# Kernel optimization log

Hardware: AMD Instinct MI355X
Metric: run time of the kernel (lower is better)

Reference implementation:

```python
import jax, jax.numpy as jnp
import numpy as np

IN_FT = 256
OUT_FT = 256


def setup_inputs() -> dict:
    key = jax.random.key(0)
    k1, k2, k3 = jax.random.split(key, 3)
    B, N = 4, 4096
    seq = jax.random.normal(k1, (B, N, IN_FT), dtype=jnp.float32)
    adj = jax.random.uniform(k2, (B, N, N), dtype=jnp.float32)
    # Xavier-uniform fc weight [out_ft, in_ft], bias zeros
    limit = float(np.sqrt(6.0 / (IN_FT + OUT_FT)))
    W = jax.random.uniform(k3, (OUT_FT, IN_FT), minval=-limit, maxval=limit, dtype=jnp.float32)
    b = jnp.zeros((OUT_FT,), dtype=jnp.float32)
    alpha = jnp.array(0.25, dtype=jnp.float32)  # PReLU shared parameter
    return {"seq": seq, "adj": adj, "W": W, "b": b, "alpha": alpha}


def reference(seq, adj, W, b, alpha):
    # Linear projection: [B, N, out_ft]
    h = jnp.einsum("bni,oi->bno", seq, W) + b
    # Neighbor aggregation (dense bmm path): [B, N, N] @ [B, N, out_ft]
    h = jnp.einsum("bnm,bmo->bno", adj, h)
    # PReLU with shared alpha
    return jnp.where(h > 0, h, alpha * h)
```

## Files before the change

### kernel.cpp

```cpp
#include <hip/hip_runtime.h>
#include <hip/hip_bf16.h>

#define NSEQ 4096
#define FT 256
#define BK 64
#define NT (NSEQ / BK)

typedef __attribute__((ext_vector_type(8))) short bf16x8;
typedef __attribute__((ext_vector_type(4))) float f32x4;

__device__ __forceinline__ ushort f2bf(float f) {
  __hip_bfloat16 h = __float2bfloat16(f);
  return *reinterpret_cast<const ushort*>(&h);
}

__device__ __forceinline__ int swz(int row, int byteInRow) {
  return row * 128 + (byteInRow ^ ((row & 7) << 4));
}

__device__ __forceinline__ void mma_step(const char* lAp, const char* lBp,
                                         int lane, int wm, int wn,
                                         f32x4 acc[2][4]) {
  const int r16 = lane & 15;
  const int g16 = (lane >> 4) * 16;
#pragma unroll
  for (int kk = 0; kk < 2; ++kk) {
    const int kb = kk * 64 + g16;
    bf16x8 a[2], b[4];
#pragma unroll
    for (int mi = 0; mi < 2; ++mi) {
      const int row = wm * 32 + mi * 16 + r16;
      a[mi] = *reinterpret_cast<const bf16x8*>(lAp + swz(row, kb));
    }
#pragma unroll
    for (int ni = 0; ni < 4; ++ni) {
      const int row = wn * 64 + ni * 16 + r16;
      b[ni] = *reinterpret_cast<const bf16x8*>(lBp + swz(row, kb));
    }
#pragma unroll
    for (int mi = 0; mi < 2; ++mi)
#pragma unroll
      for (int ni = 0; ni < 4; ++ni)
        acc[mi][ni] = __builtin_amdgcn_mfma_f32_16x16x32_bf16(a[mi], b[ni],
                                                             acc[mi][ni], 0, 0, 0);
  }
}

__global__ __launch_bounds__(512) void linear_kernel(
    const float* __restrict__ seq, const float* __restrict__ W,
    const float* __restrict__ bias, ushort* __restrict__ hT) {
  __shared__ __align__(16) ushort lA[2][64 * 64];
  __shared__ __align__(16) ushort lB[2][256 * 64];

  const int tid = threadIdx.x;
  const int lane = tid & 63;
  const int wid = tid >> 6;
  const int wm = wid >> 2, wn = wid & 3;
  const int m0 = blockIdx.x * 64;

  const int ar = tid >> 4, ac = tid & 15;

  f32x4 rA[2];
  f32x4 rB[8];

  auto gload = [&](int t) {
    const int k0 = t * BK;
#pragma unroll
    for (int p = 0; p < 2; ++p)
      rA[p] = *reinterpret_cast<const f32x4*>(
          seq + (size_t)(m0 + ar + p * 32) * FT + k0 + ac * 4);
#pragma unroll
    for (int p = 0; p < 8; ++p)
      rB[p] = *reinterpret_cast<const f32x4*>(
          W + (size_t)(ar + p * 32) * FT + k0 + ac * 4);
  };
  auto lwrite = [&](int buf) {
    char* lAp = (char*)lA[buf];
    char* lBp = (char*)lB[buf];
#pragma unroll
    for (int p = 0; p < 2; ++p) {
      ushort4 u = make_ushort4(f2bf(rA[p][0]), f2bf(rA[p][1]), f2bf(rA[p][2]), f2bf(rA[p][3]));
      *reinterpret_cast<ushort4*>(lAp + swz(ar + p * 32, ac * 8)) = u;
    }
#pragma unroll
    for (int p = 0; p < 8; ++p) {
      ushort4 u = make_ushort4(f2bf(rB[p][0]), f2bf(rB[p][1]), f2bf(rB[p][2]), f2bf(rB[p][3]));
      *reinterpret_cast<ushort4*>(lBp + swz(ar + p * 32, ac * 8)) = u;
    }
  };

  f32x4 acc[2][4];
  const f32x4 zero = {0.f, 0.f, 0.f, 0.f};
#pragma unroll
  for (int mi = 0; mi < 2; ++mi)
#pragma unroll
    for (int ni = 0; ni < 4; ++ni) acc[mi][ni] = zero;

  gload(0);
  lwrite(0);
  const int NTA = FT / BK;
  for (int t = 0; t < NTA; ++t) {
    const int cur = t & 1;
    __syncthreads();
    if (t + 1 < NTA) gload(t + 1);
    mma_step((const char*)lA[cur], (const char*)lB[cur], lane, wm, wn, acc);
    if (t + 1 < NTA) lwrite(cur ^ 1);
  }

#pragma unroll
  for (int mi = 0; mi < 2; ++mi) {
    const int grow = m0 + wm * 32 + mi * 16 + ((lane >> 4) << 2);
    const int batch = grow >> 12;
    const int n = grow & (NSEQ - 1);
#pragma unroll
    for (int ni = 0; ni < 4; ++ni) {
      const int o = wn * 64 + ni * 16 + (lane & 15);
      const float bo = bias[o];
      ushort4 u;
      u.x = f2bf(acc[mi][ni][0] + bo);
      u.y = f2bf(acc[mi][ni][1] + bo);
      u.z = f2bf(acc[mi][ni][2] + bo);
      u.w = f2bf(acc[mi][ni][3] + bo);
      *reinterpret_cast<ushort4*>(hT + (size_t)(batch * FT + o) * NSEQ + n) = u;
    }
  }
}

__global__ __launch_bounds__(512) void bmm_prelu_kernel(
    const float* __restrict__ adj, const ushort* __restrict__ hT,
    const float* __restrict__ alphaP, float* __restrict__ out) {
  __shared__ __align__(16) ushort lA[2][64 * 64];
  __shared__ __align__(16) ushort lB[4][256 * 64];

  const int tid = threadIdx.x;
  const int lane = tid & 63;
  const int wid = tid >> 6;
  const int wm = wid >> 2, wn = wid & 3;

  const int bid = blockIdx.x;
  const int sbid = (bid & 7) * 32 + (bid >> 3);
  const int batch = sbid >> 6;
  const int m0 = (sbid & 63) * 64;

  const float* adjB = adj + (size_t)batch * NSEQ * NSEQ + (size_t)m0 * NSEQ;
  const ushort* hTB = hT + (size_t)batch * FT * NSEQ;

  const int ar = tid >> 4, ac = tid & 15;
  const int brow = wid * 8 + (lane >> 3);
  const int bg = (lane & 7) ^ (lane >> 3);

  f32x4 rA0[2], rA1[2], rA2[2], rA3[2];

  f32x4 acc[2][4];
  const f32x4 zero = {0.f, 0.f, 0.f, 0.f};
#pragma unroll
  for (int mi = 0; mi < 2; ++mi)
#pragma unroll
    for (int ni = 0; ni < 4; ++ni) acc[mi][ni] = zero;

  auto issueA = [&](int t, f32x4* r) {
    const int k0 = t * BK;
#pragma unroll
    for (int p = 0; p < 2; ++p)
      r[p] = *reinterpret_cast<const f32x4*>(
          adjB + (size_t)(ar + p * 32) * NSEQ + k0 + ac * 4);
  };
  auto issueB = [&](int t, int ib) {
    const int k0 = t * BK;
#pragma unroll
    for (int p = 0; p < 4; ++p) {
      const ushort* gp = hTB + (size_t)(p * 64 + brow) * NSEQ + k0 + bg * 8;
      ushort* lp = &lB[ib][p * 4096 + wid * 512];
      __builtin_amdgcn_global_load_lds(
          (const __attribute__((address_space(1))) void*)gp,
          (__attribute__((address_space(3))) void*)lp, 16, 0, 0);
    }
  };
  auto writeA = [&](const f32x4* r, int ia) {
    char* lAp = (char*)lA[ia];
#pragma unroll
    for (int p = 0; p < 2; ++p) {
      ushort4 u = make_ushort4(f2bf(r[p][0]), f2bf(r[p][1]), f2bf(r[p][2]), f2bf(r[p][3]));
      *reinterpret_cast<ushort4*>(lAp + swz(ar + p * 32, ac * 8)) = u;
    }
  };

  issueA(0, rA0);
  issueB(0, 0);
  issueA(1, rA1);
  issueB(1, 1);
  issueA(2, rA2);
  issueB(2, 2);
  asm volatile("s_waitcnt vmcnt(16)" ::: "memory");
  writeA(rA0, 0);
  asm volatile("s_waitcnt vmcnt(12) lgkmcnt(0)" ::: "memory");
  __builtin_amdgcn_s_barrier();
  __builtin_amdgcn_sched_barrier(0);

  auto body = [&](int t, f32x4* rIss, const f32x4* rWr,
                  int ibIss, int ibRd, int iaRd, int iaWr) {
    issueA(t + 3, rIss);
    issueB(t + 3, ibIss);
    __builtin_amdgcn_s_setprio(1);
    mma_step((const char*)lA[iaRd], (const char*)lB[ibRd], lane, wm, wn, acc);
    __builtin_amdgcn_s_setprio(0);
    asm volatile("s_waitcnt vmcnt(12)" ::: "memory");
    writeA(rWr, iaWr);
    asm volatile("s_waitcnt lgkmcnt(0)" ::: "memory");
    __builtin_amdgcn_s_barrier();
    __builtin_amdgcn_sched_barrier(0);
  };

  for (int j = 0; j < 15; ++j) {
    body(j * 4 + 0, rA3, rA1, 3, 0, 0, 1);
    body(j * 4 + 1, rA0, rA2, 0, 1, 1, 0);
    body(j * 4 + 2, rA1, rA3, 1, 2, 0, 1);
    body(j * 4 + 3, rA2, rA0, 2, 3, 1, 0);
  }
  body(60, rA3, rA1, 3, 0, 0, 1);
  {
    __builtin_amdgcn_s_setprio(1);
    mma_step((const char*)lA[1], (const char*)lB[1], lane, wm, wn, acc);
    __builtin_amdgcn_s_setprio(0);
    asm volatile("s_waitcnt vmcnt(6)" ::: "memory");
    writeA(rA2, 0);
    asm volatile("s_waitcnt lgkmcnt(0)" ::: "memory");
    __builtin_amdgcn_s_barrier();
    __builtin_amdgcn_sched_barrier(0);
  }
  {
    __builtin_amdgcn_s_setprio(1);
    mma_step((const char*)lA[0], (const char*)lB[2], lane, wm, wn, acc);
    __builtin_amdgcn_s_setprio(0);
    asm volatile("s_waitcnt vmcnt(0)" ::: "memory");
    writeA(rA3, 1);
    asm volatile("s_waitcnt lgkmcnt(0)" ::: "memory");
    __builtin_amdgcn_s_barrier();
    __builtin_amdgcn_sched_barrier(0);
  }
  mma_step((const char*)lA[1], (const char*)lB[3], lane, wm, wn, acc);

  const float alpha = *alphaP;
  __syncthreads();
  float* lo = (float*)&lB[0][0];
  const int PITCH = 264;
#pragma unroll
  for (int mi = 0; mi < 2; ++mi) {
    const int rbase = wm * 32 + mi * 16 + ((lane >> 4) << 2);
#pragma unroll
    for (int ni = 0; ni < 4; ++ni) {
      const int o = wn * 64 + ni * 16 + (lane & 15);
#pragma unroll
      for (int j = 0; j < 4; ++j) {
        float v = acc[mi][ni][j];
        v = v > 0.f ? v : alpha * v;
        lo[(rbase + j) * PITCH + o] = v;
      }
    }
  }
  __syncthreads();
  float* outB = out + ((size_t)batch * NSEQ + m0) * FT;
  const int r = tid >> 3, c8 = tid & 7;
#pragma unroll
  for (int k = 0; k < 8; ++k) {
    const int g = c8 + k * 8;
    f32x4 v = *reinterpret_cast<const f32x4*>(lo + r * PITCH + g * 4);
    __builtin_nontemporal_store(v, reinterpret_cast<f32x4*>(outB + (size_t)r * FT + g * 4));
  }
}

extern "C" void kernel_launch(void* const* d_in, const int* in_sizes, int n_in,
                              void* d_out, int out_size, void* d_ws, size_t ws_size,
                              hipStream_t stream) {
  const float* seq = (const float*)d_in[0];
  const float* adj = (const float*)d_in[1];
  const float* W = (const float*)d_in[2];
  const float* bias = (const float*)d_in[3];
  const float* alpha = (const float*)d_in[4];
  float* out = (float*)d_out;
  ushort* hT = (ushort*)d_ws;

  linear_kernel<<<256, 512, 0, stream>>>(seq, W, bias, hT);
  bmm_prelu_kernel<<<256, 512, 0, stream>>>(adj, hT, alpha, out);
}
```

Measured before the change: 90.51 us.

## Switch bmm to BK=128 tiles with double buffering instead of 4-stage BK=64

```diff
diff --git a/kernel.cpp b/kernel.cpp
--- a/kernel.cpp
+++ b/kernel.cpp
@@ -4,7 +4,8 @@
 #define NSEQ 4096
 #define FT 256
 #define BK 64
-#define NT (NSEQ / BK)
+#define BKB 128
+#define NTB (NSEQ / BKB)
 
 typedef __attribute__((ext_vector_type(8))) short bf16x8;
 typedef __attribute__((ext_vector_type(4))) float f32x4;
@@ -129,8 +130,7 @@
 __global__ __launch_bounds__(512) void bmm_prelu_kernel(
     const float* __restrict__ adj, const ushort* __restrict__ hT,
     const float* __restrict__ alphaP, float* __restrict__ out) {
-  __shared__ __align__(16) ushort lA[2][64 * 64];
-  __shared__ __align__(16) ushort lB[4][256 * 64];
+  __shared__ __align__(16) char smem[2 * 65536 + 2 * 16384];
 
   const int tid = threadIdx.x;
   const int lane = tid & 63;
@@ -145,11 +145,13 @@
   const float* adjB = adj + (size_t)batch * NSEQ * NSEQ + (size_t)m0 * NSEQ;
   const ushort* hTB = hT + (size_t)batch * FT * NSEQ;
 
-  const int ar = tid >> 4, ac = tid & 15;
-  const int brow = wid * 8 + (lane >> 3);
-  const int bg = (lane & 7) ^ (lane >> 3);
-
-  f32x4 rA0[2], rA1[2], rA2[2], rA3[2];
+  auto lB = [&](int i) -> char* { return smem + i * 65536; };
+  auto lA = [&](int i) -> char* { return smem + 131072 + i * 16384; };
+
+  const int arow = tid >> 3, ac = tid & 7;
+  const int bro = (lane >> 4);
+  const int bhalf = (lane >> 3) & 1;
+  f32x4 rS[4];
 
   f32x4 acc[2][4];
   const f32x4 zero = {0.f, 0.f, 0.f, 0.f};
@@ -158,91 +160,105 @@
 #pragma unroll
     for (int ni = 0; ni < 4; ++ni) acc[mi][ni] = zero;
 
-  auto issueA = [&](int t, f32x4* r) {
-    const int k0 = t * BK;
-#pragma unroll
-    for (int p = 0; p < 2; ++p)
-      r[p] = *reinterpret_cast<const f32x4*>(
-          adjB + (size_t)(ar + p * 32) * NSEQ + k0 + ac * 4);
+  auto issueA = [&](int t) {
+    const int k0 = t * BKB;
+#pragma unroll
+    for (int q = 0; q < 4; ++q)
+      rS[q] = *reinterpret_cast<const f32x4*>(
+          adjB + (size_t)arow * NSEQ + k0 + ac * 16 + q * 4);
   };
   auto issueB = [&](int t, int ib) {
-    const int k0 = t * BK;
-#pragma unroll
-    for (int p = 0; p < 4; ++p) {
-      const ushort* gp = hTB + (size_t)(p * 64 + brow) * NSEQ + k0 + bg * 8;
-      ushort* lp = &lB[ib][p * 4096 + wid * 512];
+    const int k0 = t * BKB;
+#pragma unroll
+    for (int p = 0; p < 8; ++p) {
+      const int grow = wid * 32 + p * 4 + bro;
+      const int gsrc = (lane & 7) ^ (((p & 1) * 4 + bro) & 7);
+      const ushort* gp = hTB + (size_t)grow * NSEQ + k0 + bhalf * 64 + gsrc * 8;
+      char* lp = lB(ib) + wid * 8192 + p * 1024;
       __builtin_amdgcn_global_load_lds(
           (const __attribute__((address_space(1))) void*)gp,
           (__attribute__((address_space(3))) void*)lp, 16, 0, 0);
     }
   };
-  auto writeA = [&](const f32x4* r, int ia) {
-    char* lAp = (char*)lA[ia];
-#pragma unroll
-    for (int p = 0; p < 2; ++p) {
-      ushort4 u = make_ushort4(f2bf(r[p][0]), f2bf(r[p][1]), f2bf(r[p][2]), f2bf(r[p][3]));
-      *reinterpret_cast<ushort4*>(lAp + swz(ar + p * 32, ac * 8)) = u;
-    }
-  };
-
-  issueA(0, rA0);
+  auto writeA = [&](int ia) {
+    char* lAp = lA(ia);
+    const int half = ac >> 2;
+#pragma unroll
+    for (int q = 0; q < 4; ++q) {
+      ushort4 u = make_ushort4(f2bf(rS[q][0]), f2bf(rS[q][1]),
+                               f2bf(rS[q][2]), f2bf(rS[q][3]));
+      const int gih = (((ac & 3) * 2 + (q >> 1)) ^ (arow & 7));
+      *reinterpret_cast<ushort4*>(lAp + arow * 256 + half * 128 + gih * 16 +
+                                  (q & 1) * 8) = u;
+    }
+  };
+  auto mma32 = [&](const char* lAp, const char* lBp) {
+    const int r16 = lane & 15;
+    const int sub = lane >> 4;
+#pragma unroll
+    for (int kk = 0; kk < 4; ++kk) {
+      const int half = kk >> 1;
+      const int gih = (((kk & 1) * 4 + sub) ^ (r16 & 7));
+      const int bofs = half * 128 + gih * 16;
+      bf16x8 a[2], b[4];
+#pragma unroll
+      for (int mi = 0; mi < 2; ++mi) {
+        const int row = wm * 32 + mi * 16 + r16;
+        a[mi] = *reinterpret_cast<const bf16x8*>(lAp + row * 256 + bofs);
+      }
+#pragma unroll
+      for (int ni = 0; ni < 4; ++ni) {
+        const int row = wn * 64 + ni * 16 + r16;
+        b[ni] = *reinterpret_cast<const bf16x8*>(lBp + row * 256 + bofs);
+      }
+#pragma unroll
+      for (int mi = 0; mi < 2; ++mi)
+#pragma unroll
+        for (int ni = 0; ni < 4; ++ni)
+          acc[mi][ni] = __builtin_amdgcn_mfma_f32_16x16x32_bf16(
+              a[mi], b[ni], acc[mi][ni], 0, 0, 0);
+    }
+  };
+
+  issueA(0);
+  __builtin_amdgcn_sched_barrier(0);
   issueB(0, 0);
-  issueA(1, rA1);
-  issueB(1, 1);
-  issueA(2, rA2);
-  issueB(2, 2);
-  asm volatile("s_waitcnt vmcnt(16)" ::: "memory");
-  writeA(rA0, 0);
-  asm volatile("s_waitcnt vmcnt(12) lgkmcnt(0)" ::: "memory");
+  __builtin_amdgcn_sched_barrier(0);
+  asm volatile("s_waitcnt vmcnt(8)" ::: "memory");
+  __builtin_amdgcn_sched_barrier(0);
+  writeA(0);
+  asm volatile("s_waitcnt vmcnt(0) lgkmcnt(0)" ::: "memory");
   __builtin_amdgcn_s_barrier();
   __builtin_amdgcn_sched_barrier(0);
 
-  auto body = [&](int t, f32x4* rIss, const f32x4* rWr,
-                  int ibIss, int ibRd, int iaRd, int iaWr) {
-    issueA(t + 3, rIss);
-    issueB(t + 3, ibIss);
+  auto body = [&](int t, int cur) {
+    issueA(t + 1);
+    __builtin_amdgcn_sched_barrier(0);
+    issueB(t + 1, cur ^ 1);
+    __builtin_amdgcn_sched_barrier(0);
     __builtin_amdgcn_s_setprio(1);
-    mma_step((const char*)lA[iaRd], (const char*)lB[ibRd], lane, wm, wn, acc);
+    mma32(lA(cur), lB(cur));
     __builtin_amdgcn_s_setprio(0);
-    asm volatile("s_waitcnt vmcnt(12)" ::: "memory");
-    writeA(rWr, iaWr);
-    asm volatile("s_waitcnt lgkmcnt(0)" ::: "memory");
+    asm volatile("s_waitcnt vmcnt(8)" ::: "memory");
+    __builtin_amdgcn_sched_barrier(0);
+    writeA(cur ^ 1);
+    asm volatile("s_waitcnt vmcnt(0) lgkmcnt(0)" ::: "memory");
     __builtin_amdgcn_s_barrier();
     __builtin_amdgcn_sched_barrier(0);
   };
 
   for (int j = 0; j < 15; ++j) {
-    body(j * 4 + 0, rA3, rA1, 3, 0, 0, 1);
-    body(j * 4 + 1, rA0, rA2, 0, 1, 1, 0);
-    body(j * 4 + 2, rA1, rA3, 1, 2, 0, 1);
-    body(j * 4 + 3, rA2, rA0, 2, 3, 1, 0);
-  }
-  body(60, rA3, rA1, 3, 0, 0, 1);
-  {
-    __builtin_amdgcn_s_setprio(1);
-    mma_step((const char*)lA[1], (const char*)lB[1], lane, wm, wn, acc);
-    __builtin_amdgcn_s_setprio(0);
-    asm volatile("s_waitcnt vmcnt(6)" ::: "memory");
-    writeA(rA2, 0);
-    asm volatile("s_waitcnt lgkmcnt(0)" ::: "memory");
-    __builtin_amdgcn_s_barrier();
-    __builtin_amdgcn_sched_barrier(0);
-  }
-  {
-    __builtin_amdgcn_s_setprio(1);
-    mma_step((const char*)lA[0], (const char*)lB[2], lane, wm, wn, acc);
-    __builtin_amdgcn_s_setprio(0);
-    asm volatile("s_waitcnt vmcnt(0)" ::: "memory");
-    writeA(rA3, 1);
-    asm volatile("s_waitcnt lgkmcnt(0)" ::: "memory");
-    __builtin_amdgcn_s_barrier();
-    __builtin_amdgcn_sched_barrier(0);
-  }
-  mma_step((const char*)lA[1], (const char*)lB[3], lane, wm, wn, acc);
+    body(2 * j, 0);
+    body(2 * j + 1, 1);
+  }
+  body(30, 0);
+  __builtin_amdgcn_s_setprio(1);
+  mma32(lA(1), lB(1));
+  __builtin_amdgcn_s_setprio(0);
 
   const float alpha = *alphaP;
   __syncthreads();
-  float* lo = (float*)&lB[0][0];
+  float* lo = (float*)smem;
   const int PITCH = 264;
 #pragma unroll
   for (int mi = 0; mi < 2; ++mi) {
```

Result: faster. 83.63 us (-7.6%).
